# Kernel tuning notes

Measured on AMD Instinct MI355X. Metric: run time of the kernel, lower is better.

## Reference

```python
import jax, jax.numpy as jnp
import numpy as np

B, S, IN, N, OUT = 4, 4096, 1024, 1024, 1024  # state_size == num_heads, head_dim = 1, hippo D = 1


def setup_inputs() -> dict:
    key = jax.random.key(0)
    ks = jax.random.split(key, 6)
    x = jax.random.normal(ks[0], (B, S, IN), dtype=jnp.float32)
    # input_projection: Linear(input_size, state_size, bias=True)
    Wi = jax.random.normal(ks[1], (IN, N), dtype=jnp.float32) / np.sqrt(IN)
    bi = jax.random.normal(ks[2], (N,), dtype=jnp.float32) * 0.01
    # state_weight (N,1,1) -> per-head scalar recurrence weight; hippo_weight (N,1) -> per-head scalar
    w = jax.random.normal(ks[3], (N,), dtype=jnp.float32)
    u = jax.random.normal(ks[4], (N,), dtype=jnp.float32)
    # output_projection: Linear(state_size, output_size, bias=False)
    Wo = jax.random.normal(ks[5], (N, OUT), dtype=jnp.float32) / np.sqrt(N)
    input_state = jnp.zeros((B, N), dtype=jnp.float32)         # (B, N, H=1) squeezed
    hippo_state = jnp.zeros((B, N, 1, 1), dtype=jnp.float32)   # (B, N, H=1, D=1)
    return {"x": x, "Wi": Wi, "bi": bi, "w": w, "u": u, "Wo": Wo,
            "input_state": input_state, "hippo_state": hippo_state}


def reference(x, Wi, bi, w, u, Wo, input_state, hippo_state):
    # input projection then split into N heads of dim 1 -> [B, S, N]
    xp = jnp.einsum("bsi,in->bsn", x, Wi) + bi
    # hippo cross-term: (hippo_state @ hippo_weight) with H=D=1 -> scalar per (b, n).
    # hippo_state is never updated inside the recurrence (torch path), so this is constant over time.
    hippo_term = hippo_state[..., 0, 0] * u  # [B, N]

    def step(h, xt):
        # h_t = tanh(h_{t-1} * w + x_t + hippo_term)   (per-head scalar recurrence, H=1)
        h = jnp.tanh(h * w + xt + hippo_term)
        return h, h

    xs = jnp.swapaxes(xp, 0, 1)  # [S, B, N]
    last_state, ys = jax.lax.scan(step, input_state, xs)
    states = jnp.swapaxes(ys, 0, 1)  # [B, S, N]
    out = jnp.einsum("bsn,no->bso", states, Wo)  # output_projection (no bias)
    output_state = last_state.reshape(B, -1)     # input[:, -1] flattened over (N, H)
    return out, output_state
```

## Files before the change

### kernel.cpp

```cpp
#include <hip/hip_runtime.h>
#include <hip/hip_bf16.h>

using bf16x8 = __attribute__((ext_vector_type(8))) short;
using f32x4  = __attribute__((ext_vector_type(4))) float;

extern "C" __device__ float __ocml_native_exp2_f32(float);

static constexpr int Bc = 4, Sc = 4096, INc = 1024, Nc = 1024, OUTc = 1024;
static constexpr int Mc = Bc * Sc;
#define K2LE 2.8853900817779268f

__device__ __forceinline__ unsigned short f2b(float f) {
    return __builtin_bit_cast(unsigned short, __float2bfloat16(f));
}
__device__ __forceinline__ float b2f(unsigned short s) {
    unsigned int u = (unsigned int)s << 16;
    return __builtin_bit_cast(float, u);
}

__global__ __launch_bounds__(256) void split2(const float* __restrict__ in,
                                              unsigned short* __restrict__ hi,
                                              unsigned short* __restrict__ lo, int n4) {
    int i = blockIdx.x * blockDim.x + threadIdx.x;
    if (i >= n4) return;
    float4 v = reinterpret_cast<const float4*>(in)[i];
    ushort4 h, l;
    h.x = f2b(v.x); l.x = f2b(v.x - b2f(h.x));
    h.y = f2b(v.y); l.y = f2b(v.y - b2f(h.y));
    h.z = f2b(v.z); l.z = f2b(v.z - b2f(h.z));
    h.w = f2b(v.w); l.w = f2b(v.w - b2f(h.w));
    reinterpret_cast<ushort4*>(hi)[i] = h;
    reinterpret_cast<ushort4*>(lo)[i] = l;
}

template<bool LO>
__global__ __launch_bounds__(256) void tr_split(const float* __restrict__ in,
                                                unsigned short* __restrict__ oh,
                                                unsigned short* __restrict__ ol, int R, int C) {
    __shared__ float t[32][33];
    int c0 = blockIdx.x * 32, r0 = blockIdx.y * 32;
    for (int i = threadIdx.y; i < 32; i += 8)
        t[i][threadIdx.x] = in[(size_t)(r0 + i) * C + c0 + threadIdx.x];
    __syncthreads();
    for (int i = threadIdx.y; i < 32; i += 8) {
        float v = t[threadIdx.x][i];
        unsigned short h = f2b(v);
        size_t idx = (size_t)(c0 + i) * R + r0 + threadIdx.x;
        oh[idx] = h;
        if (LO) ol[idx] = f2b(v - b2f(h));
    }
}

__global__ __launch_bounds__(256) void gemm3_bt(const unsigned short* __restrict__ Ah,
                                                const unsigned short* __restrict__ Al,
                                                const unsigned short* __restrict__ Bh,
                                                const unsigned short* __restrict__ Bl,
                                                float* __restrict__ C, int N, int K,
                                                const float* __restrict__ bi,
                                                const float* __restrict__ u,
                                                const float* __restrict__ hs,
                                                const float* __restrict__ wv) {
    constexpr int BM = 128, BN = 128, BK = 64;
    __shared__ alignas(16) unsigned short Ash[BM * BK];
    __shared__ alignas(16) unsigned short Asl[BM * BK];
    __shared__ alignas(16) unsigned short Bsh[BN * BK];
    __shared__ alignas(16) unsigned short Bsl[BN * BK];
    const int nb = N >> 7;
    const int bm = blockIdx.x / nb, bn = blockIdx.x % nb;
    const int tid = threadIdx.x;
    const int w = tid >> 6, l = tid & 63;
    const int wr = w >> 1, wc = w & 1;
    const int r = l & 15, g4 = l >> 4;
    const int lrow = l >> 3, lcol = (l & 7) * 8;

    f32x4 acc[4][4] = {};

    const size_t aoff = (size_t)bm * BM * K;
    const size_t boff = (size_t)bn * BN * K;

    for (int k0 = 0; k0 < K; k0 += BK) {
        __syncthreads();
#pragma unroll
        for (int i = 0; i < 4; i++) {
            size_t grow = (size_t)((w * 4 + i) * 8 + lrow) * K + (k0 + lcol);
            int ldst = (w * 4 + i) * 512;
            __builtin_amdgcn_global_load_lds(
                (const __attribute__((address_space(1))) void*)(Ah + aoff + grow),
                (__attribute__((address_space(3))) void*)(Ash + ldst), 16, 0, 0);
            __builtin_amdgcn_global_load_lds(
                (const __attribute__((address_space(1))) void*)(Al + aoff + grow),
                (__attribute__((address_space(3))) void*)(Asl + ldst), 16, 0, 0);
            __builtin_amdgcn_global_load_lds(
                (const __attribute__((address_space(1))) void*)(Bh + boff + grow),
                (__attribute__((address_space(3))) void*)(Bsh + ldst), 16, 0, 0);
            __builtin_amdgcn_global_load_lds(
                (const __attribute__((address_space(1))) void*)(Bl + boff + grow),
                (__attribute__((address_space(3))) void*)(Bsl + ldst), 16, 0, 0);
        }
        __syncthreads();
#pragma unroll
        for (int kk = 0; kk < BK; kk += 32) {
            bf16x8 ah[4], al[4], bh[4], bl[4];
#pragma unroll
            for (int m = 0; m < 4; m++) {
                int off = (wr * 64 + m * 16 + r) * BK + kk + g4 * 8;
                ah[m] = *reinterpret_cast<const bf16x8*>(Ash + off);
                al[m] = *reinterpret_cast<const bf16x8*>(Asl + off);
            }
#pragma unroll
            for (int n = 0; n < 4; n++) {
                int off = (wc * 64 + n * 16 + r) * BK + kk + g4 * 8;
                bh[n] = *reinterpret_cast<const bf16x8*>(Bsh + off);
                bl[n] = *reinterpret_cast<const bf16x8*>(Bsl + off);
            }
#pragma unroll
            for (int m = 0; m < 4; m++)
#pragma unroll
                for (int n = 0; n < 4; n++) {
                    acc[m][n] = __builtin_amdgcn_mfma_f32_16x16x32_bf16(ah[m], bh[n], acc[m][n], 0, 0, 0);
                    acc[m][n] = __builtin_amdgcn_mfma_f32_16x16x32_bf16(ah[m], bl[n], acc[m][n], 0, 0, 0);
                    acc[m][n] = __builtin_amdgcn_mfma_f32_16x16x32_bf16(al[m], bh[n], acc[m][n], 0, 0, 0);
                }
        }
    }

    const int bbase = ((bm * BM) / Sc) * Nc;
#pragma unroll
    for (int m = 0; m < 4; m++) {
        int row = bm * BM + wr * 64 + m * 16 + g4 * 4;
#pragma unroll
        for (int n = 0; n < 4; n++) {
            int col = bn * BN + wc * 64 + n * 16 + r;
            float extra = bi[col] + hs[bbase + col] * u[col] + wv[col];
#pragma unroll
            for (int q = 0; q < 4; q++)
                C[(size_t)(row + q) * N + col] = (acc[m][n][q] + extra) * K2LE;
        }
    }
}

__global__ __launch_bounds__(256) void gemm_bt(const unsigned short* __restrict__ A,
                                               const unsigned short* __restrict__ BT,
                                               float* __restrict__ C, int N, int K) {
    constexpr int BM = 128, BN = 128, BK = 64;
    __shared__ alignas(16) unsigned short As[BM * BK];
    __shared__ alignas(16) unsigned short Bs[BN * BK];
    const int nb = N >> 7;
    const int bm = blockIdx.x / nb, bn = blockIdx.x % nb;
    const int tid = threadIdx.x;
    const int w = tid >> 6, l = tid & 63;
    const int wr = w >> 1, wc = w & 1;
    const int r = l & 15, g4 = l >> 4;
    const int lrow = l >> 3, lcol = (l & 7) * 8;

    f32x4 acc[4][4] = {};

    const unsigned short* Ab = A + (size_t)bm * BM * K;
    const unsigned short* Bb = BT + (size_t)bn * BN * K;

    for (int k0 = 0; k0 < K; k0 += BK) {
        __syncthreads();
#pragma unroll
        for (int i = 0; i < 4; i++) {
            const unsigned short* g = Ab + (size_t)((w * 4 + i) * 8 + lrow) * K + (k0 + lcol);
            __builtin_amdgcn_global_load_lds(
                (const __attribute__((address_space(1))) void*)g,
                (__attribute__((address_space(3))) void*)(As + (w * 4 + i) * 512), 16, 0, 0);
        }
#pragma unroll
        for (int i = 0; i < 4; i++) {
            const unsigned short* g = Bb + (size_t)((w * 4 + i) * 8 + lrow) * K + (k0 + lcol);
            __builtin_amdgcn_global_load_lds(
                (const __attribute__((address_space(1))) void*)g,
                (__attribute__((address_space(3))) void*)(Bs + (w * 4 + i) * 512), 16, 0, 0);
        }
        __syncthreads();
#pragma unroll
        for (int kk = 0; kk < BK; kk += 32) {
            bf16x8 af[4], bfr[4];
#pragma unroll
            for (int m = 0; m < 4; m++)
                af[m] = *reinterpret_cast<const bf16x8*>(As + (wr * 64 + m * 16 + r) * BK + kk + g4 * 8);
#pragma unroll
            for (int n = 0; n < 4; n++)
                bfr[n] = *reinterpret_cast<const bf16x8*>(Bs + (wc * 64 + n * 16 + r) * BK + kk + g4 * 8);
#pragma unroll
            for (int m = 0; m < 4; m++)
#pragma unroll
                for (int n = 0; n < 4; n++)
                    acc[m][n] = __builtin_amdgcn_mfma_f32_16x16x32_bf16(af[m], bfr[n], acc[m][n], 0, 0, 0);
        }
    }

#pragma unroll
    for (int m = 0; m < 4; m++) {
        int row = bm * BM + wr * 64 + m * 16 + g4 * 4;
#pragma unroll
        for (int n = 0; n < 4; n++) {
            int col = bn * BN + wc * 64 + n * 16 + r;
#pragma unroll
            for (int q = 0; q < 4; q++)
                C[(size_t)(row + q) * N + col] = acc[m][n][q];
        }
    }
}

static constexpr int SROW = 68;

template<bool PREF>
__device__ __forceinline__ void sblk(const float* __restrict__ xrow,
                                     float (&cur)[32], float (&nxt)[32],
                                     float* __restrict__ hbl, int tblk, float nw2, float& rr) {
#pragma unroll
    for (int d = 0; d < 32; d++) {
        if (PREF) nxt[d] = xrow[(size_t)(tblk + 32 + d) << 10];
        float z = fmaf(nw2, rr, cur[d]);
        float e = __ocml_native_exp2_f32(z);
        rr = __builtin_amdgcn_rcpf(e + 1.f);
        hbl[d * SROW] = rr;
    }
    asm volatile("s_waitcnt lgkmcnt(0)" ::: "memory");
    __builtin_amdgcn_s_barrier();
}

__device__ __forceinline__ unsigned int pk2(float a, float b) {
    return ((unsigned int)f2b(fmaf(-2.f, b, 1.f)) << 16) | f2b(fmaf(-2.f, a, 1.f));
}

__device__ __forceinline__ void drain(const float* __restrict__ buf, int tblk,
                                      unsigned short* __restrict__ srow, int n0, int l) {
    __builtin_amdgcn_s_barrier();
    asm volatile("" ::: "memory");
    int row8 = l >> 3, cg = l & 7;
#pragma unroll
    for (int i = 0; i < 4; i++) {
        int row = i * 8 + row8;
        float4 a = *reinterpret_cast<const float4*>(&buf[row * SROW + cg * 8]);
        float4 b = *reinterpret_cast<const float4*>(&buf[row * SROW + cg * 8 + 4]);
        uint4 v = { pk2(a.x, a.y), pk2(a.z, a.w), pk2(b.x, b.y), pk2(b.z, b.w) };
        *reinterpret_cast<uint4*>(&srow[((size_t)(tblk + row) << 10) + n0 + cg * 8]) = v;
    }
}

__global__ __launch_bounds__(128) void scan4(const float* __restrict__ xp,
                                             const float* __restrict__ w,
                                             const float* __restrict__ h0,
                                             unsigned short* __restrict__ states,
                                             float* __restrict__ out_state) {
    __shared__ alignas(16) float hb[2][32 * SROW];
    const int l = threadIdx.x & 63;
    const int wave = threadIdx.x >> 6;
    const int b = blockIdx.x >> 4;
    const int n0 = (blockIdx.x & 15) * 64;

    if (wave == 0) {
        const int tid = blockIdx.x * 64 + l;
        const int n = tid & (Nc - 1);
        float nw2 = w[n] * (-2.f * K2LE);
        float rr = 0.5f - 0.5f * h0[tid];
        const float* xrow = xp + ((size_t)b << 22) + n;
        float* hbl0 = &hb[0][l];
        float* hbl1 = &hb[1][l];

        float xa[32], xb[32];
#pragma unroll
        for (int d = 0; d < 32; d++) xa[d] = xrow[(size_t)d << 10];

        int t = 0;
        for (; t + 64 < Sc; t += 64) {
            sblk<true>(xrow, xa, xb, hbl0, t, nw2, rr);
            sblk<true>(xrow, xb, xa, hbl1, t + 32, nw2, rr);
        }
        sblk<true >(xrow, xa, xb, hbl0, t, nw2, rr);
        sblk<false>(xrow, xb, xa, hbl1, t + 32, nw2, rr);
        out_state[tid] = fmaf(-2.f, rr, 1.f);
    } else {
        unsigned short* srow = states + ((size_t)b << 22);
        for (int t = 0; t < Sc; t += 64) {
            drain(hb[0], t, srow, n0, l);
            drain(hb[1], t + 32, srow, n0, l);
        }
    }
}

extern "C" void kernel_launch(void* const* d_in, const int* in_sizes, int n_in,
                              void* d_out, int out_size, void* d_ws, size_t ws_size,
                              hipStream_t stream) {
    const float* x  = (const float*)d_in[0];
    const float* Wi = (const float*)d_in[1];
    const float* bi = (const float*)d_in[2];
    const float* w  = (const float*)d_in[3];
    const float* u  = (const float*)d_in[4];
    const float* Wo = (const float*)d_in[5];
    const float* h0 = (const float*)d_in[6];
    const float* hs = (const float*)d_in[7];
    float* out = (float*)d_out;
    float* out_state = out + (size_t)Mc * OUTc;
    float* xp = out;

    char* ws = (char*)d_ws;
    unsigned short* xh   = (unsigned short*)ws;
    unsigned short* xl   = (unsigned short*)(ws + 33554432);
    unsigned short* WiTh = (unsigned short*)(ws + 67108864);
    unsigned short* WiTl = (unsigned short*)(ws + 69206016);
    unsigned short* WoT  = (unsigned short*)(ws + 71303168);
    unsigned short* states = xh;

    split2<<<(Mc * INc / 4 + 255) / 256, 256, 0, stream>>>(x, xh, xl, Mc * INc / 4);
    dim3 tb(32, 8);
    tr_split<true ><<<dim3(Nc / 32, INc / 32), tb, 0, stream>>>(Wi, WiTh, WiTl, INc, Nc);
    tr_split<false><<<dim3(OUTc / 32, Nc / 32), tb, 0, stream>>>(Wo, WoT, nullptr, Nc, OUTc);

    gemm3_bt<<<(Mc / 128) * (Nc / 128), 256, 0, stream>>>(xh, xl, WiTh, WiTl, xp, Nc, INc, bi, u, hs, w);
    scan4<<<64, 128, 0, stream>>>(xp, w, h0, states, out_state);
    gemm_bt<<<(Mc / 128) * (OUTc / 128), 256, 0, stream>>>(states, WoT, out, OUTc, Nc);
}
```

Before: 290.0 us.

## Switch GEMMs from bf16 split to fp16 with two-term input-side split

Both GEMMs now use fp16 MFMA instead of bf16. The input projection drops from three MFMAs per tile step (hi*hi, hi*lo, lo*hi) to two (xh*W, xl*W), with only x split into hi/lo, which removes the Wi low-part buffer, its loads and one third of the matrix work. The two GEMM kernels are merged into one template, and the block index is remapped in an XCD-aware way to improve L2 locality. Accuracy now depends on fp16 range and precision for the weights and the packed states, which is a risk if values overflow or need more mantissa than fp16 keeps.

```diff
diff --git a/kernel.cpp b/kernel.cpp
--- a/kernel.cpp
+++ b/kernel.cpp
@@ -1,8 +1,8 @@
 #include <hip/hip_runtime.h>
 #include <hip/hip_bf16.h>
 
-using bf16x8 = __attribute__((ext_vector_type(8))) short;
-using f32x4  = __attribute__((ext_vector_type(4))) float;
+using f16x8 = __attribute__((ext_vector_type(8))) _Float16;
+using f32x4 = __attribute__((ext_vector_type(4))) float;
 
 extern "C" __device__ float __ocml_native_exp2_f32(float);
 
@@ -10,63 +10,56 @@
 static constexpr int Mc = Bc * Sc;
 #define K2LE 2.8853900817779268f
 
-__device__ __forceinline__ unsigned short f2b(float f) {
-    return __builtin_bit_cast(unsigned short, __float2bfloat16(f));
-}
-__device__ __forceinline__ float b2f(unsigned short s) {
-    unsigned int u = (unsigned int)s << 16;
-    return __builtin_bit_cast(float, u);
-}
-
-__global__ __launch_bounds__(256) void split2(const float* __restrict__ in,
-                                              unsigned short* __restrict__ hi,
-                                              unsigned short* __restrict__ lo, int n4) {
+__device__ __forceinline__ unsigned short f2h(float f) {
+    return __builtin_bit_cast(unsigned short, (_Float16)f);
+}
+__device__ __forceinline__ float h2f(unsigned short s) {
+    return (float)__builtin_bit_cast(_Float16, s);
+}
+
+__global__ __launch_bounds__(256) void split2h(const float* __restrict__ in,
+                                               unsigned short* __restrict__ hi,
+                                               unsigned short* __restrict__ lo, int n4) {
     int i = blockIdx.x * blockDim.x + threadIdx.x;
     if (i >= n4) return;
     float4 v = reinterpret_cast<const float4*>(in)[i];
     ushort4 h, l;
-    h.x = f2b(v.x); l.x = f2b(v.x - b2f(h.x));
-    h.y = f2b(v.y); l.y = f2b(v.y - b2f(h.y));
-    h.z = f2b(v.z); l.z = f2b(v.z - b2f(h.z));
-    h.w = f2b(v.w); l.w = f2b(v.w - b2f(h.w));
+    h.x = f2h(v.x); l.x = f2h(v.x - h2f(h.x));
+    h.y = f2h(v.y); l.y = f2h(v.y - h2f(h.y));
+    h.z = f2h(v.z); l.z = f2h(v.z - h2f(h.z));
+    h.w = f2h(v.w); l.w = f2h(v.w - h2f(h.w));
     reinterpret_cast<ushort4*>(hi)[i] = h;
     reinterpret_cast<ushort4*>(lo)[i] = l;
 }
 
-template<bool LO>
-__global__ __launch_bounds__(256) void tr_split(const float* __restrict__ in,
-                                                unsigned short* __restrict__ oh,
-                                                unsigned short* __restrict__ ol, int R, int C) {
+__global__ __launch_bounds__(256) void tr_h(const float* __restrict__ in,
+                                            unsigned short* __restrict__ out, int R, int C) {
     __shared__ float t[32][33];
     int c0 = blockIdx.x * 32, r0 = blockIdx.y * 32;
     for (int i = threadIdx.y; i < 32; i += 8)
         t[i][threadIdx.x] = in[(size_t)(r0 + i) * C + c0 + threadIdx.x];
     __syncthreads();
-    for (int i = threadIdx.y; i < 32; i += 8) {
-        float v = t[threadIdx.x][i];
-        unsigned short h = f2b(v);
-        size_t idx = (size_t)(c0 + i) * R + r0 + threadIdx.x;
-        oh[idx] = h;
-        if (LO) ol[idx] = f2b(v - b2f(h));
-    }
-}
-
-__global__ __launch_bounds__(256) void gemm3_bt(const unsigned short* __restrict__ Ah,
-                                                const unsigned short* __restrict__ Al,
-                                                const unsigned short* __restrict__ Bh,
-                                                const unsigned short* __restrict__ Bl,
-                                                float* __restrict__ C, int N, int K,
-                                                const float* __restrict__ bi,
-                                                const float* __restrict__ u,
-                                                const float* __restrict__ hs,
-                                                const float* __restrict__ wv) {
+    for (int i = threadIdx.y; i < 32; i += 8)
+        out[(size_t)(c0 + i) * R + r0 + threadIdx.x] = f2h(t[threadIdx.x][i]);
+}
+
+template<int MODE>
+__global__ __launch_bounds__(256) void gemm_h(const unsigned short* __restrict__ Ah,
+                                              const unsigned short* __restrict__ Al,
+                                              const unsigned short* __restrict__ BT,
+                                              float* __restrict__ C, int N, int K,
+                                              const float* __restrict__ bi,
+                                              const float* __restrict__ u,
+                                              const float* __restrict__ hs,
+                                              const float* __restrict__ wv) {
     constexpr int BM = 128, BN = 128, BK = 64;
     __shared__ alignas(16) unsigned short Ash[BM * BK];
-    __shared__ alignas(16) unsigned short Asl[BM * BK];
-    __shared__ alignas(16) unsigned short Bsh[BN * BK];
-    __shared__ alignas(16) unsigned short Bsl[BN * BK];
+    __shared__ alignas(16) unsigned short Asl[MODE ? BM * BK : 1];
+    __shared__ alignas(16) unsigned short Bs[BN * BK];
     const int nb = N >> 7;
-    const int bm = blockIdx.x / nb, bn = blockIdx.x % nb;
+    const int cpx = (int)gridDim.x >> 3;
+    const int wg = (blockIdx.x & 7) * cpx + (blockIdx.x >> 3);
+    const int bm = wg / nb, bn = wg % nb;
     const int tid = threadIdx.x;
     const int w = tid >> 6, l = tid & 63;
     const int wr = w >> 1, wc = w & 1;
@@ -87,120 +80,53 @@
             __builtin_amdgcn_global_load_lds(
                 (const __attribute__((address_space(1))) void*)(Ah + aoff + grow),
                 (__attribute__((address_space(3))) void*)(Ash + ldst), 16, 0, 0);
+            if (MODE)
+                __builtin_amdgcn_global_load_lds(
+                    (const __attribute__((address_space(1))) void*)(Al + aoff + grow),
+                    (__attribute__((address_space(3))) void*)(Asl + ldst), 16, 0, 0);
             __builtin_amdgcn_global_load_lds(
-                (const __attribute__((address_space(1))) void*)(Al + aoff + grow),
-                (__attribute__((address_space(3))) void*)(Asl + ldst), 16, 0, 0);
-            __builtin_amdgcn_global_load_lds(
-                (const __attribute__((address_space(1))) void*)(Bh + boff + grow),
-                (__attribute__((address_space(3))) void*)(Bsh + ldst), 16, 0, 0);
-            __builtin_amdgcn_global_load_lds(
-                (const __attribute__((address_space(1))) void*)(Bl + boff + grow),
-                (__attribute__((address_space(3))) void*)(Bsl + ldst), 16, 0, 0);
+                (const __attribute__((address_space(1))) void*)(BT + boff + grow),
+                (__attribute__((address_space(3))) void*)(Bs + ldst), 16, 0, 0);
         }
         __syncthreads();
 #pragma unroll
         for (int kk = 0; kk < BK; kk += 32) {
-            bf16x8 ah[4], al[4], bh[4], bl[4];
+            f16x8 ah[4], al[4], bf[4];
 #pragma unroll
             for (int m = 0; m < 4; m++) {
                 int off = (wr * 64 + m * 16 + r) * BK + kk + g4 * 8;
-                ah[m] = *reinterpret_cast<const bf16x8*>(Ash + off);
-                al[m] = *reinterpret_cast<const bf16x8*>(Asl + off);
+                ah[m] = *reinterpret_cast<const f16x8*>(Ash + off);
+                if (MODE) al[m] = *reinterpret_cast<const f16x8*>(Asl + off);
             }
 #pragma unroll
-            for (int n = 0; n < 4; n++) {
-                int off = (wc * 64 + n * 16 + r) * BK + kk + g4 * 8;
-                bh[n] = *reinterpret_cast<const bf16x8*>(Bsh + off);
-                bl[n] = *reinterpret_cast<const bf16x8*>(Bsl + off);
-            }
+            for (int n = 0; n < 4; n++)
+                bf[n] = *reinterpret_cast<const f16x8*>(Bs + (wc * 64 + n * 16 + r) * BK + kk + g4 * 8);
 #pragma unroll
             for (int m = 0; m < 4; m++)
 #pragma unroll
                 for (int n = 0; n < 4; n++) {
-                    acc[m][n] = __builtin_amdgcn_mfma_f32_16x16x32_bf16(ah[m], bh[n], acc[m][n], 0, 0, 0);
-                    acc[m][n] = __builtin_amdgcn_mfma_f32_16x16x32_bf16(ah[m], bl[n], acc[m][n], 0, 0, 0);
-                    acc[m][n] = __builtin_amdgcn_mfma_f32_16x16x32_bf16(al[m], bh[n], acc[m][n], 0, 0, 0);
+                    acc[m][n] = __builtin_amdgcn_mfma_f32_16x16x32_f16(ah[m], bf[n], acc[m][n], 0, 0, 0);
+                    if (MODE)
+                        acc[m][n] = __builtin_amdgcn_mfma_f32_16x16x32_f16(al[m], bf[n], acc[m][n], 0, 0, 0);
                 }
         }
     }
 
-    const int bbase = ((bm * BM) / Sc) * Nc;
+    const int bbase = MODE ? ((bm * BM) / Sc) * Nc : 0;
 #pragma unroll
     for (int m = 0; m < 4; m++) {
         int row = bm * BM + wr * 64 + m * 16 + g4 * 4;
 #pragma unroll
         for (int n = 0; n < 4; n++) {
             int col = bn * BN + wc * 64 + n * 16 + r;
-            float extra = bi[col] + hs[bbase + col] * u[col] + wv[col];
-#pragma unroll
-            for (int q = 0; q < 4; q++)
-                C[(size_t)(row + q) * N + col] = (acc[m][n][q] + extra) * K2LE;
-        }
-    }
-}
-
-__global__ __launch_bounds__(256) void gemm_bt(const unsigned short* __restrict__ A,
-                                               const unsigned short* __restrict__ BT,
-                                               float* __restrict__ C, int N, int K) {
-    constexpr int BM = 128, BN = 128, BK = 64;
-    __shared__ alignas(16) unsigned short As[BM * BK];
-    __shared__ alignas(16) unsigned short Bs[BN * BK];
-    const int nb = N >> 7;
-    const int bm = blockIdx.x / nb, bn = blockIdx.x % nb;
-    const int tid = threadIdx.x;
-    const int w = tid >> 6, l = tid & 63;
-    const int wr = w >> 1, wc = w & 1;
-    const int r = l & 15, g4 = l >> 4;
-    const int lrow = l >> 3, lcol = (l & 7) * 8;
-
-    f32x4 acc[4][4] = {};
-
-    const unsigned short* Ab = A + (size_t)bm * BM * K;
-    const unsigned short* Bb = BT + (size_t)bn * BN * K;
-
-    for (int k0 = 0; k0 < K; k0 += BK) {
-        __syncthreads();
-#pragma unroll
-        for (int i = 0; i < 4; i++) {
-            const unsigned short* g = Ab + (size_t)((w * 4 + i) * 8 + lrow) * K + (k0 + lcol);
-            __builtin_amdgcn_global_load_lds(
-                (const __attribute__((address_space(1))) void*)g,
-                (__attribute__((address_space(3))) void*)(As + (w * 4 + i) * 512), 16, 0, 0);
-        }
-#pragma unroll
-        for (int i = 0; i < 4; i++) {
-            const unsigned short* g = Bb + (size_t)((w * 4 + i) * 8 + lrow) * K + (k0 + lcol);
-            __builtin_amdgcn_global_load_lds(
-                (const __attribute__((address_space(1))) void*)g,
-                (__attribute__((address_space(3))) void*)(Bs + (w * 4 + i) * 512), 16, 0, 0);
-        }
-        __syncthreads();
-#pragma unroll
-        for (int kk = 0; kk < BK; kk += 32) {
-            bf16x8 af[4], bfr[4];
-#pragma unroll
-            for (int m = 0; m < 4; m++)
-                af[m] = *reinterpret_cast<const bf16x8*>(As + (wr * 64 + m * 16 + r) * BK + kk + g4 * 8);
-#pragma unroll
-            for (int n = 0; n < 4; n++)
-                bfr[n] = *reinterpret_cast<const bf16x8*>(Bs + (wc * 64 + n * 16 + r) * BK + kk + g4 * 8);
-#pragma unroll
-            for (int m = 0; m < 4; m++)
-#pragma unroll
-                for (int n = 0; n < 4; n++)
-                    acc[m][n] = __builtin_amdgcn_mfma_f32_16x16x32_bf16(af[m], bfr[n], acc[m][n], 0, 0, 0);
-        }
-    }
-
-#pragma unroll
-    for (int m = 0; m < 4; m++) {
-        int row = bm * BM + wr * 64 + m * 16 + g4 * 4;
-#pragma unroll
-        for (int n = 0; n < 4; n++) {
-            int col = bn * BN + wc * 64 + n * 16 + r;
-#pragma unroll
-            for (int q = 0; q < 4; q++)
-                C[(size_t)(row + q) * N + col] = acc[m][n][q];
+            float extra = 0.f;
+            if (MODE) extra = bi[col] + hs[bbase + col] * u[col] + wv[col];
+#pragma unroll
+            for (int q = 0; q < 4; q++) {
+                float v = acc[m][n][q];
+                if (MODE) v = (v + extra) * K2LE;
+                C[(size_t)(row + q) * N + col] = v;
+            }
         }
     }
 }
@@ -224,7 +150,7 @@
 }
 
 __device__ __forceinline__ unsigned int pk2(float a, float b) {
-    return ((unsigned int)f2b(fmaf(-2.f, b, 1.f)) << 16) | f2b(fmaf(-2.f, a, 1.f));
+    return ((unsigned int)f2h(fmaf(-2.f, b, 1.f)) << 16) | f2h(fmaf(-2.f, a, 1.f));
 }
 
 __device__ __forceinline__ void drain(const float* __restrict__ buf, int tblk,
@@ -299,19 +225,19 @@
     float* xp = out;
 
     char* ws = (char*)d_ws;
-    unsigned short* xh   = (unsigned short*)ws;
-    unsigned short* xl   = (unsigned short*)(ws + 33554432);
-    unsigned short* WiTh = (unsigned short*)(ws + 67108864);
-    unsigned short* WiTl = (unsigned short*)(ws + 69206016);
-    unsigned short* WoT  = (unsigned short*)(ws + 71303168);
+    unsigned short* xh  = (unsigned short*)ws;
+    unsigned short* xl  = (unsigned short*)(ws + 33554432);
+    unsigned short* WiT = (unsigned short*)(ws + 67108864);
+    unsigned short* WoT = (unsigned short*)(ws + 69206016);
     unsigned short* states = xh;
 
-    split2<<<(Mc * INc / 4 + 255) / 256, 256, 0, stream>>>(x, xh, xl, Mc * INc / 4);
+    split2h<<<(Mc * INc / 4 + 255) / 256, 256, 0, stream>>>(x, xh, xl, Mc * INc / 4);
     dim3 tb(32, 8);
-    tr_split<true ><<<dim3(Nc / 32, INc / 32), tb, 0, stream>>>(Wi, WiTh, WiTl, INc, Nc);
-    tr_split<false><<<dim3(OUTc / 32, Nc / 32), tb, 0, stream>>>(Wo, WoT, nullptr, Nc, OUTc);
-
-    gemm3_bt<<<(Mc / 128) * (Nc / 128), 256, 0, stream>>>(xh, xl, WiTh, WiTl, xp, Nc, INc, bi, u, hs, w);
+    tr_h<<<dim3(Nc / 32, INc / 32), tb, 0, stream>>>(Wi, WiT, INc, Nc);
+    tr_h<<<dim3(OUTc / 32, Nc / 32), tb, 0, stream>>>(Wo, WoT, Nc, OUTc);
+
+    gemm_h<1><<<(Mc / 128) * (Nc / 128), 256, 0, stream>>>(xh, xl, WiT, xp, Nc, INc, bi, u, hs, w);
     scan4<<<64, 128, 0, stream>>>(xp, w, h0, states, out_state);
-    gemm_bt<<<(Mc / 128) * (OUTc / 128), 256, 0, stream>>>(states, WoT, out, OUTc, Nc);
-}
+    gemm_h<0><<<(Mc / 128) * (OUTc / 128), 256, 0, stream>>>(states, nullptr, WoT, out, OUTc, Nc,
+                                                             nullptr, nullptr, nullptr, nullptr);
+}
```

Result: faster. 256.9 us (-11.4%).
